# Optimization experiments

Measured on AMD Instinct MI355X. Metric: run time of the kernel, lower is better.

## Reference

```python
import jax, jax.numpy as jnp
import numpy as np

B, M, EMB, K = 32768, 2048, 128, 8
TAU = 0.3

def setup_inputs() -> dict:
    key = jax.random.key(0)
    ks = jax.random.split(key, 6)
    return {
        "Gl_cur": jax.random.normal(ks[0], (B, 2), dtype=jnp.float32),
        "ancL": jax.random.normal(ks[1], (B, M, 2), dtype=jnp.float32),
        "W1": jax.random.normal(ks[2], (EMB, 2), dtype=jnp.float32) * 0.5,
        "b1": jax.random.normal(ks[3], (EMB,), dtype=jnp.float32) * 0.1,
        "W2": jax.random.normal(ks[4], (EMB, EMB), dtype=jnp.float32) * (1.0 / np.sqrt(EMB)),
        "b2": jax.random.normal(ks[5], (EMB,), dtype=jnp.float32) * 0.1,
    }

def reference(Gl_cur, ancL, W1, b1, W2, b2):
    # pairwise squared distances: [B, M]
    d2 = jnp.sum((ancL - Gl_cur[:, None, :]) ** 2, axis=-1)
    # top-k nearest anchors (topk of -d2, as in torch code)
    vals, idxs = jax.lax.top_k(-d2, K)              # vals: [B,K] (negated d2)
    topA = jnp.take_along_axis(ancL, idxs[:, :, None], axis=1)  # [B,K,2]
    # 2-layer GELU MLP (exact/erf GELU, torch default); dropout inactive in eval
    h1 = jax.nn.gelu(jnp.einsum('bkc,ec->bke', topA, W1) + b1, approximate=False)
    topE = jax.nn.gelu(jnp.einsum('bke,fe->bkf', h1, W2) + b2, approximate=False)
    # softmax combine: w = softmax(vals / -tau) = softmax(d2_top / tau), faithful to source
    w = jax.nn.softmax(vals / (-TAU), axis=1)       # [B,K]
    return jnp.sum(topE * w[:, :, None], axis=1)    # [B, EMB]
```

## Files before the change

### kernel.cpp

```cpp
#include <hip/hip_runtime.h>
#include <hip/hip_bf16.h>
#include <math.h>

#define NB   32768
#define NM   2048
#define NEMB 128
#define NK   8
#define TAU  0.3f
#define FLT_BIG 3.402823466e38f

typedef __attribute__((ext_vector_type(8))) short bf16x8;
typedef __attribute__((ext_vector_type(4))) float f32x4;

__device__ __forceinline__ float gelu_tanh(float x) {
    const float x2 = x * x;
    const float u  = fmaf(0.044715f, x2, 1.0f);
    const float a  = x * u * (-2.3022082f);
    const float e  = __builtin_amdgcn_exp2f(a);
    const float r  = __builtin_amdgcn_rcpf(e + 1.0f);
    return x * r;
}
__device__ __forceinline__ unsigned pack2(float lo, float hi) {
    __hip_bfloat162 b = __float22bfloat162_rn(make_float2(lo, hi));
    return *reinterpret_cast<unsigned*>(&b);
}

template<int CTRL>
__device__ __forceinline__ unsigned dpp_umin(unsigned v) {
    const unsigned t = (unsigned)__builtin_amdgcn_update_dpp(0, (int)v, CTRL, 0xF, 0xF, true);
    return v < t ? v : t;
}
template<int CTRL>
__device__ __forceinline__ float dpp_fadd(float v) {
    const float t = __int_as_float(__builtin_amdgcn_update_dpp(0, __float_as_int(v), CTRL, 0xF, 0xF, true));
    return v + t;
}

__device__ __forceinline__ void ins3(float (&bd)[3], unsigned (&bp)[3], float d, unsigned p) {
    const bool c0 = d < bd[0], c1 = d < bd[1], c2 = d < bd[2];
    const float n2 = __builtin_amdgcn_fmed3f(d, bd[1], bd[2]);
    const float n1 = __builtin_amdgcn_fmed3f(d, bd[0], bd[1]);
    const float n0 = fminf(d, bd[0]);
    bp[2] = c1 ? bp[1] : (c2 ? p : bp[2]);
    bp[1] = c0 ? bp[0] : (c1 ? p : bp[1]);
    bp[0] = c0 ? p : bp[0];
    bd[2] = n2; bd[1] = n1; bd[0] = n0;
}

template<int DEPTH>
__device__ __forceinline__ int ext_round(float (&ld)[DEPTH], unsigned (&lp)[DEPTH],
                                         float &td, unsigned &tp, const int lane) {
    const unsigned key = __float_as_uint(ld[0]);
    unsigned m = key;
    m = dpp_umin<0xB1>(m);  m = dpp_umin<0x4E>(m);
    m = dpp_umin<0x141>(m); m = dpp_umin<0x140>(m);
    { unsigned t = __shfl_xor(m, 16); m = m < t ? m : t;
      t = __shfl_xor(m, 32);          m = m < t ? m : t; }
    const unsigned long long mk = __ballot(key == m);
    const int src = __ffsll(mk) - 1;
    td = __uint_as_float(m);
    tp = __shfl(lp[0], src);
    if (lane == src) {
#pragma unroll
        for (int j = 0; j < DEPTH - 1; ++j) { ld[j] = ld[j + 1]; lp[j] = lp[j + 1]; }
        ld[DEPTH - 1] = FLT_BIG;
        return 1;
    }
    return 0;
}

template<int DEPTH>
__device__ __forceinline__ int extract8(float (&ld)[DEPTH], unsigned (&lp)[DEPTH],
                                        float (&td)[8], unsigned (&tp)[8], const int lane) {
    int pops = 0;
#pragma unroll
    for (int k = 0; k < 8; ++k) pops += ext_round<DEPTH>(ld, lp, td[k], tp[k], lane);
    return pops;
}

__device__ __forceinline__ void fallback_row(const f32x4* a4, const float2 g,
                                             float (&td)[8], unsigned (&tp)[8], const int lane) {
    float    fd[8];
    unsigned fp[8];
#pragma unroll
    for (int i = 0; i < 8; ++i) { fd[i] = FLT_BIG; fp[i] = 0u; }
    for (int it = 0; it < 16; ++it) {
        const f32x4 vv = a4[it * 64 + lane];
#pragma unroll
        for (int h = 0; h < 2; ++h) {
            const float ax = h ? vv.z : vv.x;
            const float ay = h ? vv.w : vv.y;
            const float ddx = ax - g.x, ddy = ay - g.y;
            const float d = __fadd_rn(__fmul_rn(ddx, ddx), __fmul_rn(ddy, ddy));
            if (d < fd[7]) {
                const unsigned p = pack2(ax, ay);
#pragma unroll
                for (int j = 7; j >= 1; --j) {
                    const bool s1 = fd[j - 1] > d;
                    const bool s2 = fd[j] > d;
                    const float    nd = s1 ? fd[j - 1] : (s2 ? d : fd[j]);
                    const unsigned np = s1 ? fp[j - 1] : (s2 ? p : fp[j]);
                    fd[j] = nd; fp[j] = np;
                }
                if (fd[0] > d) { fd[0] = d; fp[0] = p; }
            }
        }
    }
    (void)extract8<8>(fd, fp, td, tp, lane);
}

__global__ void __launch_bounds__(512, 6) fused_anchor_mlp(
    const float* __restrict__ Gl, const float* __restrict__ ancL,
    const float* __restrict__ W1, const float* __restrict__ b1,
    const float* __restrict__ W2, const float* __restrict__ b2,
    float* __restrict__ out)
{
    __shared__ uint4  w2s[2048];
    __shared__ uint4  h1s4[1024];
    __shared__ float4 b2s4[32];
    __shared__ float  wts[8][8];

    const int tid  = threadIdx.x;
    const int wave = tid >> 6;
    const int lane = tid & 63;
    const int pair = wave >> 1;
    const int half = wave & 1;
    const int rowbase = blockIdx.x << 3;
    const int row  = rowbase + wave;

    {
        const float4* w2f = reinterpret_cast<const float4*>(W2);
        for (int i = tid; i < 2048; i += 512) {
            const float4 lo = w2f[i * 2], hi = w2f[i * 2 + 1];
            uint4 u;
            u.x = pack2(lo.x, lo.y); u.y = pack2(lo.z, lo.w);
            u.z = pack2(hi.x, hi.y); u.w = pack2(hi.z, hi.w);
            w2s[(i & ~15) | ((i & 15) ^ ((i >> 4) & 7))] = u;
        }
        if (tid < 32) b2s4[tid] = reinterpret_cast<const float4*>(b2)[tid];
    }

    const float2 g = reinterpret_cast<const float2*>(Gl)[row];
    const f32x4* a4 = reinterpret_cast<const f32x4*>(ancL) + (size_t)row * (NM / 2);

    float    bd[3];
    unsigned bp[3];
#pragma unroll
    for (int i = 0; i < 3; ++i) { bd[i] = FLT_BIG; bp[i] = 0u; }

    f32x4 bufA[3], bufB[3];
#pragma unroll
    for (int j = 0; j < 3; ++j) {
        bufA[j] = a4[j * 128 + lane];
        bufB[j] = a4[j * 128 + 64 + lane];
    }

#pragma unroll
    for (int it = 0; it < 8; ++it) {
        const int slot = it % 3;
        const f32x4 vA = bufA[slot];
        const f32x4 vB = bufB[slot];
        if (it + 3 < 8) {
            bufA[slot] = a4[(it + 3) * 128 + lane];
            bufB[slot] = a4[(it + 3) * 128 + 64 + lane];
        }
        const float dxA0 = vA.x - g.x, dyA0 = vA.y - g.y;
        const float dxA1 = vA.z - g.x, dyA1 = vA.w - g.y;
        const float dA0 = __fadd_rn(__fmul_rn(dxA0, dxA0), __fmul_rn(dyA0, dyA0));
        const float dA1 = __fadd_rn(__fmul_rn(dxA1, dxA1), __fmul_rn(dyA1, dyA1));
        const float dxB0 = vB.x - g.x, dyB0 = vB.y - g.y;
        const float dxB1 = vB.z - g.x, dyB1 = vB.w - g.y;
        const float dB0 = __fadd_rn(__fmul_rn(dxB0, dxB0), __fmul_rn(dyB0, dyB0));
        const float dB1 = __fadd_rn(__fmul_rn(dxB1, dxB1), __fmul_rn(dyB1, dyB1));
        ins3(bd, bp, dA0, pack2(vA.x, vA.y));
        ins3(bd, bp, dA1, pack2(vA.z, vA.w));
        ins3(bd, bp, dB0, pack2(vB.x, vB.y));
        ins3(bd, bp, dB1, pack2(vB.z, vB.w));
    }

    float    td[8];
    unsigned tp[8];
    const int pops = extract8<3>(bd, bp, td, tp, lane);

    if (__ballot(pops == 3)) fallback_row(a4, g, td, tp, lane);

    const float mx = td[7];
    float ek[8], ssum = 0.f;
#pragma unroll
    for (int k = 0; k < 8; ++k) { ek[k] = __expf((td[k] - mx) * (1.0f / TAU)); ssum += ek[k]; }
    const float inv = 1.0f / ssum;
    float wv = 0.f;
#pragma unroll
    for (int k = 0; k < 8; ++k) wv = (lane == k) ? ek[k] * inv : wv;
    if (lane < 8) wts[wave][lane] = wv;

    const float4 w1v = reinterpret_cast<const float4*>(W1)[lane];
    const float2 b1v = reinterpret_cast<const float2*>(b1)[lane];
    unsigned* h1w = reinterpret_cast<unsigned*>(h1s4 + (pair << 8));
#pragma unroll
    for (int k = 0; k < 8; ++k) {
        const unsigned pk = tp[k];
        const float ax = __uint_as_float(pk << 16);
        const float ay = __uint_as_float(pk & 0xFFFF0000u);
        const float x0 = fmaf(ax, w1v.x, fmaf(ay, w1v.y, b1v.x));
        const float x1 = fmaf(ax, w1v.z, fmaf(ay, w1v.w, b1v.y));
        const int r = (half << 3) + k;
        h1w[(r << 6) + ((((lane >> 2) ^ k) << 2) | (lane & 3))] = pack2(gelu_tanh(x0), gelu_tanh(x1));
    }
    __syncthreads();

    const uint4* h1b = h1s4 + (pair << 8);
    const int bslot = lane >> 4, bxor = lane & 7, brow = (lane & 15) * 16;
    bf16x8 bq0 = __builtin_bit_cast(bf16x8, h1b[brow + (( 0 + bslot) ^ bxor)]);
    bf16x8 bq1 = __builtin_bit_cast(bf16x8, h1b[brow + (( 4 + bslot) ^ bxor)]);
    bf16x8 bq2 = __builtin_bit_cast(bf16x8, h1b[brow + (( 8 + bslot) ^ bxor)]);
    bf16x8 bq3 = __builtin_bit_cast(bf16x8, h1b[brow + ((12 + bslot) ^ bxor)]);

    const float wsel = wts[(pair << 1) | ((lane >> 3) & 1)][lane & 7];

#pragma unroll 2
    for (int i = 0; i < 4; ++i) {
        const int ft = (half << 2) + i;
        const int arow = (ft * 16 + (lane & 15)) * 16;
        f32x4 acc = {0.f, 0.f, 0.f, 0.f};
        acc = __builtin_amdgcn_mfma_f32_16x16x32_bf16(
                  __builtin_bit_cast(bf16x8, w2s[arow + (( 0 + bslot) ^ bxor)]), bq0, acc, 0, 0, 0);
        acc = __builtin_amdgcn_mfma_f32_16x16x32_bf16(
                  __builtin_bit_cast(bf16x8, w2s[arow + (( 4 + bslot) ^ bxor)]), bq1, acc, 0, 0, 0);
        acc = __builtin_amdgcn_mfma_f32_16x16x32_bf16(
                  __builtin_bit_cast(bf16x8, w2s[arow + (( 8 + bslot) ^ bxor)]), bq2, acc, 0, 0, 0);
        acc = __builtin_amdgcn_mfma_f32_16x16x32_bf16(
                  __builtin_bit_cast(bf16x8, w2s[arow + ((12 + bslot) ^ bxor)]), bq3, acc, 0, 0, 0);

        const float4 b2v = b2s4[ft * 4 + (lane >> 4)];
        float s0 = gelu_tanh(acc[0] + b2v.x) * wsel;
        float s1 = gelu_tanh(acc[1] + b2v.y) * wsel;
        float s2 = gelu_tanh(acc[2] + b2v.z) * wsel;
        float s3 = gelu_tanh(acc[3] + b2v.w) * wsel;
        s0 = dpp_fadd<0xB1>(s0); s0 = dpp_fadd<0x4E>(s0); s0 = dpp_fadd<0x141>(s0);
        s1 = dpp_fadd<0xB1>(s1); s1 = dpp_fadd<0x4E>(s1); s1 = dpp_fadd<0x141>(s1);
        s2 = dpp_fadd<0xB1>(s2); s2 = dpp_fadd<0x4E>(s2); s2 = dpp_fadd<0x141>(s2);
        s3 = dpp_fadd<0xB1>(s3); s3 = dpp_fadd<0x4E>(s3); s3 = dpp_fadd<0x141>(s3);
        if ((lane & 7) == 0) {
            const int which = (lane >> 3) & 1;
            const size_t ob = (size_t)(rowbase + (pair << 1) + which) * NEMB
                              + ft * 16 + ((lane >> 4) << 2);
            *reinterpret_cast<float4*>(&out[ob]) = make_float4(s0, s1, s2, s3);
        }
    }
}

extern "C" void kernel_launch(void* const* d_in, const int* in_sizes, int n_in,
                              void* d_out, int out_size, void* d_ws, size_t ws_size,
                              hipStream_t stream)
{
    const float* Gl  = (const float*)d_in[0];
    const float* anc = (const float*)d_in[1];
    const float* W1  = (const float*)d_in[2];
    const float* b1  = (const float*)d_in[3];
    const float* W2  = (const float*)d_in[4];
    const float* b2  = (const float*)d_in[5];
    float* outp = (float*)d_out;

    fused_anchor_mlp<<<NB / 8, 512, 0, stream>>>(Gl, anc, W1, b1, W2, b2, outp);
}
```

Before: 132.8 us.

## Spread each row's top-k scan across all block waves with LDS merge

Instead of each wave scanning its own row's 2048 anchors, all 512 threads stream the block's 8 rows contiguously. Each thread keeps a per-row top-3 list, and per-wave top-8 candidates are merged through shared memory into each row's final top-8. Fallback detection becomes per row and per wave-chunk. The goal is more coalesced, fully contiguous loads and better memory-level parallelism. The cost is 24 tracked candidates per thread plus an extra block-wide barrier, so launch bounds drop occupancy from 6 to 5.

```diff
diff --git a/kernel.cpp b/kernel.cpp
--- a/kernel.cpp
+++ b/kernel.cpp
@@ -109,7 +109,7 @@
     (void)extract8<8>(fd, fp, td, tp, lane);
 }
 
-__global__ void __launch_bounds__(512, 6) fused_anchor_mlp(
+__global__ void __launch_bounds__(512, 5) fused_anchor_mlp(
     const float* __restrict__ Gl, const float* __restrict__ ancL,
     const float* __restrict__ W1, const float* __restrict__ b1,
     const float* __restrict__ W2, const float* __restrict__ b2,
@@ -119,6 +119,8 @@
     __shared__ uint4  h1s4[1024];
     __shared__ float4 b2s4[32];
     __shared__ float  wts[8][8];
+    __shared__ uint2  lmerge[8][8][8];
+    __shared__ int    fbflags[8];
 
     const int tid  = threadIdx.x;
     const int wave = tid >> 6;
@@ -126,7 +128,6 @@
     const int pair = wave >> 1;
     const int half = wave & 1;
     const int rowbase = blockIdx.x << 3;
-    const int row  = rowbase + wave;
 
     {
         const float4* w2f = reinterpret_cast<const float4*>(W2);
@@ -140,49 +141,68 @@
         if (tid < 32) b2s4[tid] = reinterpret_cast<const float4*>(b2)[tid];
     }
 
-    const float2 g = reinterpret_cast<const float2*>(Gl)[row];
-    const f32x4* a4 = reinterpret_cast<const f32x4*>(ancL) + (size_t)row * (NM / 2);
-
-    float    bd[3];
-    unsigned bp[3];
-#pragma unroll
-    for (int i = 0; i < 3; ++i) { bd[i] = FLT_BIG; bp[i] = 0u; }
-
-    f32x4 bufA[3], bufB[3];
-#pragma unroll
-    for (int j = 0; j < 3; ++j) {
-        bufA[j] = a4[j * 128 + lane];
-        bufB[j] = a4[j * 128 + 64 + lane];
-    }
-
-#pragma unroll
-    for (int it = 0; it < 8; ++it) {
-        const int slot = it % 3;
-        const f32x4 vA = bufA[slot];
-        const f32x4 vB = bufB[slot];
-        if (it + 3 < 8) {
-            bufA[slot] = a4[(it + 3) * 128 + lane];
-            bufB[slot] = a4[(it + 3) * 128 + 64 + lane];
-        }
-        const float dxA0 = vA.x - g.x, dyA0 = vA.y - g.y;
-        const float dxA1 = vA.z - g.x, dyA1 = vA.w - g.y;
-        const float dA0 = __fadd_rn(__fmul_rn(dxA0, dxA0), __fmul_rn(dyA0, dyA0));
-        const float dA1 = __fadd_rn(__fmul_rn(dxA1, dxA1), __fmul_rn(dyA1, dyA1));
-        const float dxB0 = vB.x - g.x, dyB0 = vB.y - g.y;
-        const float dxB1 = vB.z - g.x, dyB1 = vB.w - g.y;
-        const float dB0 = __fadd_rn(__fmul_rn(dxB0, dxB0), __fmul_rn(dyB0, dyB0));
-        const float dB1 = __fadd_rn(__fmul_rn(dxB1, dxB1), __fmul_rn(dyB1, dyB1));
-        ins3(bd, bp, dA0, pack2(vA.x, vA.y));
-        ins3(bd, bp, dA1, pack2(vA.z, vA.w));
-        ins3(bd, bp, dB0, pack2(vB.x, vB.y));
-        ins3(bd, bp, dB1, pack2(vB.z, vB.w));
-    }
-
+    const float2* Gl2 = reinterpret_cast<const float2*>(Gl);
+    float2 g8[8];
+#pragma unroll
+    for (int r = 0; r < 8; ++r) g8[r] = Gl2[rowbase + r];
+
+    const f32x4* ab = reinterpret_cast<const f32x4*>(ancL) + (size_t)rowbase * (NM / 2);
+
+    float    bd[8][3];
+    unsigned bp[8][3];
+#pragma unroll
+    for (int r = 0; r < 8; ++r)
+#pragma unroll
+        for (int i = 0; i < 3; ++i) { bd[r][i] = FLT_BIG; bp[r][i] = 0u; }
+
+    f32x4 buf[2];
+    buf[0] = ab[tid];
+    buf[1] = ab[512 + tid];
+
+#pragma unroll
+    for (int s = 0; s < 16; ++s) {
+        const f32x4 v = buf[s & 1];
+        if (s + 2 < 16) buf[s & 1] = ab[(s + 2) * 512 + tid];
+        const int r = s >> 1;
+        const float dx0 = v.x - g8[r].x, dy0 = v.y - g8[r].y;
+        const float dx1 = v.z - g8[r].x, dy1 = v.w - g8[r].y;
+        const float d0 = __fadd_rn(__fmul_rn(dx0, dx0), __fmul_rn(dy0, dy0));
+        const float d1 = __fadd_rn(__fmul_rn(dx1, dx1), __fmul_rn(dy1, dy1));
+        ins3(bd[r], bp[r], d0, pack2(v.x, v.y));
+        ins3(bd[r], bp[r], d1, pack2(v.z, v.w));
+    }
+
+    int fbmask = 0;
+#pragma unroll
+    for (int r = 0; r < 8; ++r) {
+        int pops = 0;
+#pragma unroll
+        for (int k = 0; k < 8; ++k) {
+            float etd; unsigned etp;
+            pops += ext_round<3>(bd[r], bp[r], etd, etp, lane);
+            if (lane == k) lmerge[r][wave][k] = make_uint2(__float_as_uint(etd), etp);
+        }
+        if (__ballot(pops == 3)) fbmask |= (1 << r);
+    }
+    if (lane == 0) fbflags[wave] = fbmask;
+    __syncthreads();
+
+    const uint2 cand = lmerge[wave][lane >> 3][lane & 7];
+    float    md[1] = { __uint_as_float(cand.x) };
+    unsigned mp[1] = { cand.y };
     float    td[8];
     unsigned tp[8];
-    const int pops = extract8<3>(bd, bp, td, tp, lane);
-
-    if (__ballot(pops == 3)) fallback_row(a4, g, td, tp, lane);
+    (void)extract8<1>(md, mp, td, tp, lane);
+
+    int allfb = 0;
+#pragma unroll
+    for (int w = 0; w < 8; ++w) allfb |= fbflags[w];
+    if ((allfb >> wave) & 1) {
+        const f32x4* aOwn = reinterpret_cast<const f32x4*>(ancL)
+                            + (size_t)(rowbase + wave) * (NM / 2);
+        const float2 gOwn = Gl2[rowbase + wave];
+        fallback_row(aOwn, gOwn, td, tp, lane);
+    }
 
     const float mx = td[7];
     float ek[8], ssum = 0.f;
```

Result: slower. 251.5 us (+89.4%).
